# Kernel tuning notes

Hardware: AMD Instinct MI355X
Metric: run time of the kernel (lower is better)

## Reference

```python
import jax, jax.numpy as jnp
from jax import lax
import numpy as np

B, HW, C = 32, 4096, 256
G = 32            # factor / groups
CG = C // G       # per-group channels = 8
EPS = 1e-5


def setup_inputs() -> dict:
    key = jax.random.key(0)
    ks = jax.random.split(key, 7)
    s = 1.0 / np.sqrt(CG)
    s3 = 1.0 / np.sqrt(CG * 9)
    return {
        "x": jax.random.normal(ks[0], (B, HW, C), dtype=jnp.float32),
        "w1": jax.random.uniform(ks[1], (CG, CG), jnp.float32, -s, s),        # conv1x1 weight (O,I)
        "b1": jax.random.uniform(ks[2], (CG,), jnp.float32, -s, s),
        "w3": jax.random.uniform(ks[3], (CG, CG, 3, 3), jnp.float32, -s3, s3),  # conv3x3 weight (O,I,kH,kW)
        "b3": jax.random.uniform(ks[4], (CG,), jnp.float32, -s3, s3),
        "gn_w": jnp.ones((CG,), jnp.float32),
        "gn_b": jnp.zeros((CG,), jnp.float32),
    }


def reference(x, w1, b1, w3, b3, gn_w, gn_b):
    b, hw, c = x.shape
    h = int(np.sqrt(hw)); w = h
    cg = c // G
    n = b * G
    # (b, hw, c) -> (b, c, h, w) -> (b*G, cg, h, w)
    gx = x.transpose(0, 2, 1).reshape(b, c, h, w).reshape(n, cg, h, w)

    # directional pooling
    x_h = gx.mean(axis=3, keepdims=True)                       # (n,cg,h,1)
    x_w = gx.mean(axis=2, keepdims=True).transpose(0, 1, 3, 2)  # (n,cg,w,1)
    cat = jnp.concatenate([x_h, x_w], axis=2)                  # (n,cg,h+w,1)
    # 1x1 conv == channel matmul
    hwm = jnp.einsum('oi,nipq->nopq', w1, cat) + b1[None, :, None, None]
    xh, xw = hwm[:, :, :h], hwm[:, :, h:]

    gated = gx * jax.nn.sigmoid(xh) * jax.nn.sigmoid(xw.transpose(0, 1, 3, 2))

    # GroupNorm(cg groups over cg channels) == per-channel norm over spatial dims
    mu = gated.mean(axis=(2, 3), keepdims=True)
    var = gated.var(axis=(2, 3), keepdims=True)
    x1 = (gated - mu) * lax.rsqrt(var + EPS) * gn_w[None, :, None, None] + gn_b[None, :, None, None]

    x2 = lax.conv_general_dilated(gx, w3, (1, 1), ((1, 1), (1, 1)),
                                  dimension_numbers=('NCHW', 'OIHW', 'NCHW')) + b3[None, :, None, None]

    x11 = jax.nn.softmax(x1.mean(axis=(2, 3)), axis=-1)[:, None, :]  # (n,1,cg)
    x21 = jax.nn.softmax(x2.mean(axis=(2, 3)), axis=-1)[:, None, :]  # (n,1,cg)
    x12 = x2.reshape(n, cg, h * w)
    x22 = x1.reshape(n, cg, h * w)

    weights = (x11 @ x12 + x21 @ x22).reshape(n, 1, h, w)
    out = (gx * jax.nn.sigmoid(weights)).reshape(b, c, h, w)
    return out.reshape(b, c, hw).transpose(0, 2, 1)
```

## Files before the change

### kernel.cpp

```cpp
#include <hip/hip_runtime.h>
#include <math.h>


#define NBLK 1024
#define NTHR 512
#define CSTR 2052
#define USTR 4104

typedef unsigned int uint;
typedef unsigned short ushort;

__device__ __forceinline__ uint pk2(float a, float b) {
    uint ua = __builtin_bit_cast(uint, a);
    uint ub = __builtin_bit_cast(uint, b);
    ua = (ua + 0x7FFFu + ((ua >> 16) & 1u)) >> 16;
    ub = (ub + 0x7FFFu + ((ub >> 16) & 1u)) >> 16;
    return ua | (ub << 16);
}
__device__ __forceinline__ float blo(uint u) { return __builtin_bit_cast(float, u << 16); }
__device__ __forceinline__ float bhi(uint u) { return __builtin_bit_cast(float, u & 0xFFFF0000u); }
__device__ __forceinline__ float bfs(ushort s) { return __builtin_bit_cast(float, ((uint)s) << 16); }
__device__ __forceinline__ float sigm(float v) { return 1.0f / (1.0f + __expf(-v)); }
__device__ __forceinline__ uint pksig(float a, float b) {
    return (uint)(a * 65535.0f + 0.5f) | ((uint)(b * 65535.0f + 0.5f) << 16);
}

__global__ __launch_bounds__(512, 4) void fused_ema_kernel(
    const float* __restrict__ x,
    const float* __restrict__ w1,
    const float* __restrict__ b1,
    const float* __restrict__ w3,
    const float* __restrict__ b3,
    const float* __restrict__ gn_w,
    const float* __restrict__ gn_b,
    float* __restrict__ out)
{
    __shared__ __align__(16) uint  gxp[8 * CSTR];
    __shared__ __align__(16) float sg[8 * 128];
    __shared__ __align__(16) float uni[2048];
    __shared__ __align__(16) float t1s[8 * 64];
    __shared__ float weff[72];
    __shared__ float Ti[8], m2s[8], Ai[8], Ci[8], x11s[8], x21s[8];
    __shared__ float wconst_s;

    const int t = threadIdx.x;
    const int bi = blockIdx.x;
    const int n = ((bi & 7) * 32 + ((bi >> 3) >> 2)) * 4 + ((bi >> 3) & 3);
    const int b = n >> 5;
    const int g = n & 31;

    {
        const float4* x4 = reinterpret_cast<const float4*>(x) + (size_t)b * 4096 * 64 + g * 2;
#pragma unroll
        for (int k = 0; k < 8; ++k) {
            int idx = k * 512 + t;
            int q = idx >> 1;
            int half = idx & 1;
            float4 v0 = x4[(size_t)q * 128 + half];
            float4 v1 = x4[(size_t)q * 128 + 64 + half];
            int ch = half * 4;
            gxp[(ch + 0) * CSTR + q] = pk2(v0.x, v1.x);
            gxp[(ch + 1) * CSTR + q] = pk2(v0.y, v1.y);
            gxp[(ch + 2) * CSTR + q] = pk2(v0.z, v1.z);
            gxp[(ch + 3) * CSTR + q] = pk2(v0.w, v1.w);
        }
    }
    __syncthreads();

    float* Rs = uni;
    float* Cs = uni + 512;

    {
        const int i = t >> 6, l = t & 63, ys = l >> 3, xb = l & 7;
        float col[8] = {0, 0, 0, 0, 0, 0, 0, 0};
        float row[8];
#pragma unroll
        for (int r = 0; r < 8; ++r) {
            const uint4 d = *reinterpret_cast<const uint4*>(
                &gxp[i * CSTR + (ys * 8 + r) * 32 + xb * 4]);
            float f0 = blo(d.x), f1 = bhi(d.x), f2 = blo(d.y), f3 = bhi(d.y);
            float f4 = blo(d.z), f5 = bhi(d.z), f6 = blo(d.w), f7 = bhi(d.w);
            row[r] = ((f0 + f1) + (f2 + f3)) + ((f4 + f5) + (f6 + f7));
            col[0] += f0; col[1] += f1; col[2] += f2; col[3] += f3;
            col[4] += f4; col[5] += f5; col[6] += f6; col[7] += f7;
        }
#pragma unroll
        for (int r = 0; r < 8; ++r) {
            float v = row[r];
            v += __shfl_xor(v, 1); v += __shfl_xor(v, 2); v += __shfl_xor(v, 4);
            if (xb == 0) Rs[i * 64 + ys * 8 + r] = v;
        }
        float tot = 0.f;
#pragma unroll
        for (int j = 0; j < 8; ++j) {
            float c = col[j];
            c += __shfl_xor(c, 8); c += __shfl_xor(c, 16); c += __shfl_xor(c, 32);
            if (ys == 0) Cs[i * 64 + xb * 8 + j] = c;
            tot += c;
        }
        tot += __shfl_xor(tot, 1); tot += __shfl_xor(tot, 2); tot += __shfl_xor(tot, 4);
        if (l == 0) Ti[i] = tot;
    }
    __syncthreads();

    {
        const int o = t >> 6, p = t & 63;
        float vy = b1[o], vx = b1[o];
#pragma unroll
        for (int i = 0; i < 8; ++i) {
            float wv = w1[o * 8 + i] * (1.0f / 64.0f);
            vy += wv * Rs[i * 64 + p];
            vx += wv * Cs[i * 64 + p];
        }
        sg[o * 128 + p] = sigm(vy);
        sg[o * 128 + 64 + p] = sigm(vx);
    }
    __syncthreads();

    {
        const int i = t >> 6, l = t & 63, ys = l >> 3, xb = l & 7;
        const float4 sa = *reinterpret_cast<const float4*>(&sg[i * 128 + 64 + xb * 8]);
        const float4 sb = *reinterpret_cast<const float4*>(&sg[i * 128 + 64 + xb * 8 + 4]);
        float s = 0.f, s2 = 0.f;
#pragma unroll
        for (int r = 0; r < 8; ++r) {
            const float shv = sg[i * 128 + ys * 8 + r];
            const uint4 d = *reinterpret_cast<const uint4*>(
                &gxp[i * CSTR + (ys * 8 + r) * 32 + xb * 4]);
            float g0 = blo(d.x) * shv * sa.x; s += g0; s2 += g0 * g0;
            float g1 = bhi(d.x) * shv * sa.y; s += g1; s2 += g1 * g1;
            float g2 = blo(d.y) * shv * sa.z; s += g2; s2 += g2 * g2;
            float g3 = bhi(d.y) * shv * sa.w; s += g3; s2 += g3 * g3;
            float g4 = blo(d.z) * shv * sb.x; s += g4; s2 += g4 * g4;
            float g5 = bhi(d.z) * shv * sb.y; s += g5; s2 += g5 * g5;
            float g6 = blo(d.w) * shv * sb.z; s += g6; s2 += g6 * g6;
            float g7 = bhi(d.w) * shv * sb.w; s += g7; s2 += g7 * g7;
        }
#pragma unroll
        for (int off = 32; off; off >>= 1) {
            s += __shfl_xor(s, off);
            s2 += __shfl_xor(s2, off);
        }
        if (l == 0) {
            float mu = s * (1.0f / 4096.0f);
            float var = s2 * (1.0f / 4096.0f) - mu * mu;
            float a = rsqrtf(var + 1e-5f) * gn_w[i];
            Ai[i] = a;
            Ci[i] = gn_b[i] - mu * a;
        }
    }
    if (t < 64) {
        const int o = t >> 3, i = t & 7;
        const float T = Ti[i];
        float part = 0.f;
#pragma unroll
        for (int ky = 0; ky < 3; ++ky) {
            int dy = ky - 1;
#pragma unroll
            for (int kx = 0; kx < 3; ++kx) {
                int dx = kx - 1;
                float S = T;
                int er = (dy < 0) ? 63 : 0;
                int ec = (dx < 0) ? 63 : 0;
                if (dy != 0) S -= Rs[i * 64 + er];
                if (dx != 0) S -= Cs[i * 64 + ec];
                if (dy != 0 && dx != 0) {
                    uint u = gxp[i * CSTR + er * 32 + (ec >> 1)];
                    S += (ec & 1) ? bhi(u) : blo(u);
                }
                part += w3[((o * 8 + i) * 3 + ky) * 3 + kx] * S;
            }
        }
        part += __shfl_xor(part, 1); part += __shfl_xor(part, 2); part += __shfl_xor(part, 4);
        if (i == 0) m2s[o] = part * (1.0f / 4096.0f) + b3[o];
    }
    if (t < 8) {
        float mx = m2s[0];
#pragma unroll
        for (int o = 1; o < 8; ++o) mx = fmaxf(mx, m2s[o]);
        float sum = 0.f;
#pragma unroll
        for (int o = 0; o < 8; ++o) sum += __expf(m2s[o] - mx);
        x21s[t] = __expf(m2s[t] - mx) / sum;
        float mx1 = gn_b[0];
#pragma unroll
        for (int o = 1; o < 8; ++o) mx1 = fmaxf(mx1, gn_b[o]);
        float sum1 = 0.f;
#pragma unroll
        for (int o = 0; o < 8; ++o) sum1 += __expf(gn_b[o] - mx1);
        x11s[t] = __expf(gn_b[t] - mx1) / sum1;
    }
    __syncthreads();

    if (t < 72) {
        const int i = t / 9, k = t % 9;
        float acc = 0.f;
#pragma unroll
        for (int o = 0; o < 8; ++o) acc += x11s[o] * w3[(o * 8 + i) * 9 + k];
        weff[i * 9 + k] = acc;
    }
    {
        const int i = t >> 6, y = t & 63;
        t1s[i * 64 + y] = x21s[i] * Ai[i] * sg[i * 128 + y];
    }
    if (t == 0) {
        float wc = 0.f;
#pragma unroll
        for (int o = 0; o < 8; ++o) wc += x11s[o] * b3[o] + x21s[o] * Ci[o];
        wconst_s = wc;
    }
    __syncthreads();

    {
        const int y = t >> 3, xb = t & 7;
        const ushort* gxs = reinterpret_cast<const ushort*>(gxp);
        float ws0 = wconst_s, ws1 = ws0, ws2 = ws0, ws3 = ws0;
        float ws4 = ws0, ws5 = ws0, ws6 = ws0, ws7 = ws0;
#pragma unroll
        for (int i = 0; i < 8; ++i) {
            const float t1v = t1s[i * 64 + y];
            const float4 sa = *reinterpret_cast<const float4*>(&sg[i * 128 + 64 + xb * 8]);
            const float4 sb = *reinterpret_cast<const float4*>(&sg[i * 128 + 64 + xb * 8 + 4]);
            const int xm = (xb == 0) ? 0 : (xb * 8 - 1);
            const int xp = (xb == 7) ? 63 : (xb * 8 + 8);
#pragma unroll
            for (int dy = -1; dy <= 1; ++dy) {
                const int yy = y + dy;
                if (yy < 0 || yy > 63) continue;
                const uint4 d = *reinterpret_cast<const uint4*>(
                    &gxp[i * CSTR + yy * 32 + xb * 4]);
                float f0 = blo(d.x), f1 = bhi(d.x), f2 = blo(d.y), f3 = bhi(d.y);
                float f4 = blo(d.z), f5 = bhi(d.z), f6 = blo(d.w), f7 = bhi(d.w);
                float vm = (xb == 0) ? 0.f : bfs(gxs[i * USTR + yy * 64 + xm]);
                float vp = (xb == 7) ? 0.f : bfs(gxs[i * USTR + yy * 64 + xp]);
                const float* wp = &weff[i * 9 + (dy + 1) * 3];
                const float wl = wp[0], wc = wp[1], wr = wp[2];
                ws0 += wl * vm + wc * f0 + wr * f1;
                ws1 += wl * f0 + wc * f1 + wr * f2;
                ws2 += wl * f1 + wc * f2 + wr * f3;
                ws3 += wl * f2 + wc * f3 + wr * f4;
                ws4 += wl * f3 + wc * f4 + wr * f5;
                ws5 += wl * f4 + wc * f5 + wr * f6;
                ws6 += wl * f5 + wc * f6 + wr * f7;
                ws7 += wl * f6 + wc * f7 + wr * vp;
                if (dy == 0) {
                    ws0 += t1v * sa.x * f0;  ws1 += t1v * sa.y * f1;
                    ws2 += t1v * sa.z * f2;  ws3 += t1v * sa.w * f3;
                    ws4 += t1v * sb.x * f4;  ws5 += t1v * sb.y * f5;
                    ws6 += t1v * sb.z * f6;  ws7 += t1v * sb.w * f7;
                }
            }
        }
        uint* psum = reinterpret_cast<uint*>(uni);
        const int qb = y * 32 + xb * 4;
        psum[qb + 0] = pksig(sigm(ws0), sigm(ws1));
        psum[qb + 1] = pksig(sigm(ws2), sigm(ws3));
        psum[qb + 2] = pksig(sigm(ws4), sigm(ws5));
        psum[qb + 3] = pksig(sigm(ws6), sigm(ws7));
    }
    __syncthreads();

    {
        const uint* psum = reinterpret_cast<const uint*>(uni);
        float4* out4 = reinterpret_cast<float4*>(out) + (size_t)b * 4096 * 64 + g * 2;
#pragma unroll
        for (int j = 0; j < 4; ++j) {
            const int q = j * 512 + t;
            const uint sp = psum[q];
            const float s0 = (float)(sp & 0xFFFFu) * (1.0f / 65535.0f);
            const float s1 = (float)(sp >> 16) * (1.0f / 65535.0f);
            const uint u0 = gxp[0 * CSTR + q], u1 = gxp[1 * CSTR + q];
            const uint u2 = gxp[2 * CSTR + q], u3 = gxp[3 * CSTR + q];
            const uint u4 = gxp[4 * CSTR + q], u5 = gxp[5 * CSTR + q];
            const uint u6 = gxp[6 * CSTR + q], u7 = gxp[7 * CSTR + q];
            float4 a0, a1, c0, c1;
            a0.x = blo(u0) * s0; a0.y = blo(u1) * s0; a0.z = blo(u2) * s0; a0.w = blo(u3) * s0;
            a1.x = blo(u4) * s0; a1.y = blo(u5) * s0; a1.z = blo(u6) * s0; a1.w = blo(u7) * s0;
            c0.x = bhi(u0) * s1; c0.y = bhi(u1) * s1; c0.z = bhi(u2) * s1; c0.w = bhi(u3) * s1;
            c1.x = bhi(u4) * s1; c1.y = bhi(u5) * s1; c1.z = bhi(u6) * s1; c1.w = bhi(u7) * s1;
            const size_t p0 = (size_t)q * 128;
            out4[p0] = a0;
            out4[p0 + 1] = a1;
            out4[p0 + 64] = c0;
            out4[p0 + 65] = c1;
        }
    }
}

extern "C" void kernel_launch(void* const* d_in, const int* in_sizes, int n_in,
                              void* d_out, int out_size, void* d_ws, size_t ws_size,
                              hipStream_t stream) {
    const float* x    = (const float*)d_in[0];
    const float* w1   = (const float*)d_in[1];
    const float* b1   = (const float*)d_in[2];
    const float* w3   = (const float*)d_in[3];
    const float* b3   = (const float*)d_in[4];
    const float* gn_w = (const float*)d_in[5];
    const float* gn_b = (const float*)d_in[6];
    float* out = (float*)d_out;

    hipLaunchKernelGGL(fused_ema_kernel, dim3(NBLK), dim3(NTHR), 0, stream,
                       x, w1, b1, w3, b3, gn_w, gn_b, out);
}
```

Before: 89.53 us.

## Double threads per block and fuse conv output into final store

Raises the block size from 512 to 1024 threads so each thread covers 4 pixels instead of 8 in every phase, with a two-part column-sum and GroupNorm reduction across half-blocks. The 3x3 conv phase now takes left and right neighbours via wavefront shuffles instead of extra LDS loads, and keeps the centre row's data in registers so the output is written directly. This removes the packed-sigmoid LDS round-trip, its extra barrier and the 16-bit sigmoid quantisation. It adds barriers and reduction steps. The output store pattern changes from fully contiguous rows per warp to per-pixel strided float4 writes, which may hurt coalescing.

```diff
diff --git a/kernel.cpp b/kernel.cpp
--- a/kernel.cpp
+++ b/kernel.cpp
@@ -3,12 +3,10 @@
 
 
 #define NBLK 1024
-#define NTHR 512
+#define NTHR 1024
 #define CSTR 2052
-#define USTR 4104
 
 typedef unsigned int uint;
-typedef unsigned short ushort;
 
 __device__ __forceinline__ uint pk2(float a, float b) {
     uint ua = __builtin_bit_cast(uint, a);
@@ -19,13 +17,9 @@
 }
 __device__ __forceinline__ float blo(uint u) { return __builtin_bit_cast(float, u << 16); }
 __device__ __forceinline__ float bhi(uint u) { return __builtin_bit_cast(float, u & 0xFFFF0000u); }
-__device__ __forceinline__ float bfs(ushort s) { return __builtin_bit_cast(float, ((uint)s) << 16); }
 __device__ __forceinline__ float sigm(float v) { return 1.0f / (1.0f + __expf(-v)); }
-__device__ __forceinline__ uint pksig(float a, float b) {
-    return (uint)(a * 65535.0f + 0.5f) | ((uint)(b * 65535.0f + 0.5f) << 16);
-}
-
-__global__ __launch_bounds__(512, 4) void fused_ema_kernel(
+
+__global__ __launch_bounds__(1024, 8) void fused_ema_kernel(
     const float* __restrict__ x,
     const float* __restrict__ w1,
     const float* __restrict__ b1,
@@ -37,10 +31,12 @@
 {
     __shared__ __align__(16) uint  gxp[8 * CSTR];
     __shared__ __align__(16) float sg[8 * 128];
-    __shared__ __align__(16) float uni[2048];
-    __shared__ __align__(16) float t1s[8 * 64];
+    __shared__ __align__(16) float uni[1024];
+    __shared__ __align__(16) float csp1[512];
+    __shared__ __align__(16) float t1s[512];
     __shared__ float weff[72];
     __shared__ float Ti[8], m2s[8], Ai[8], Ci[8], x11s[8], x21s[8];
+    __shared__ float sPart[16], s2Part[16];
     __shared__ float wconst_s;
 
     const int t = threadIdx.x;
@@ -52,8 +48,8 @@
     {
         const float4* x4 = reinterpret_cast<const float4*>(x) + (size_t)b * 4096 * 64 + g * 2;
 #pragma unroll
-        for (int k = 0; k < 8; ++k) {
-            int idx = k * 512 + t;
+        for (int k = 0; k < 4; ++k) {
+            int idx = k * 1024 + t;
             int q = idx >> 1;
             int half = idx & 1;
             float4 v0 = x4[(size_t)q * 128 + half];
@@ -71,83 +67,90 @@
     float* Cs = uni + 512;
 
     {
-        const int i = t >> 6, l = t & 63, ys = l >> 3, xb = l & 7;
-        float col[8] = {0, 0, 0, 0, 0, 0, 0, 0};
-        float row[8];
+        const int i = t >> 7, l = t & 127;
+        const int ys2 = l >> 4, xb2 = l & 15;
+        float c0 = 0.f, c1 = 0.f, c2 = 0.f, c3 = 0.f;
+        float rowv[8];
 #pragma unroll
         for (int r = 0; r < 8; ++r) {
-            const uint4 d = *reinterpret_cast<const uint4*>(
-                &gxp[i * CSTR + (ys * 8 + r) * 32 + xb * 4]);
+            const uint2 d = *reinterpret_cast<const uint2*>(
+                &gxp[i * CSTR + (ys2 * 8 + r) * 32 + xb2 * 2]);
             float f0 = blo(d.x), f1 = bhi(d.x), f2 = blo(d.y), f3 = bhi(d.y);
-            float f4 = blo(d.z), f5 = bhi(d.z), f6 = blo(d.w), f7 = bhi(d.w);
-            row[r] = ((f0 + f1) + (f2 + f3)) + ((f4 + f5) + (f6 + f7));
-            col[0] += f0; col[1] += f1; col[2] += f2; col[3] += f3;
-            col[4] += f4; col[5] += f5; col[6] += f6; col[7] += f7;
+            rowv[r] = (f0 + f1) + (f2 + f3);
+            c0 += f0; c1 += f1; c2 += f2; c3 += f3;
         }
 #pragma unroll
         for (int r = 0; r < 8; ++r) {
-            float v = row[r];
-            v += __shfl_xor(v, 1); v += __shfl_xor(v, 2); v += __shfl_xor(v, 4);
-            if (xb == 0) Rs[i * 64 + ys * 8 + r] = v;
-        }
-        float tot = 0.f;
-#pragma unroll
-        for (int j = 0; j < 8; ++j) {
-            float c = col[j];
-            c += __shfl_xor(c, 8); c += __shfl_xor(c, 16); c += __shfl_xor(c, 32);
-            if (ys == 0) Cs[i * 64 + xb * 8 + j] = c;
-            tot += c;
-        }
-        tot += __shfl_xor(tot, 1); tot += __shfl_xor(tot, 2); tot += __shfl_xor(tot, 4);
-        if (l == 0) Ti[i] = tot;
-    }
-    __syncthreads();
-
-    {
-        const int o = t >> 6, p = t & 63;
-        float vy = b1[o], vx = b1[o];
+            float v = rowv[r];
+            v += __shfl_xor(v, 1); v += __shfl_xor(v, 2);
+            v += __shfl_xor(v, 4); v += __shfl_xor(v, 8);
+            if (xb2 == 0) Rs[i * 64 + ys2 * 8 + r] = v;
+        }
+        c0 += __shfl_xor(c0, 16); c0 += __shfl_xor(c0, 32);
+        c1 += __shfl_xor(c1, 16); c1 += __shfl_xor(c1, 32);
+        c2 += __shfl_xor(c2, 16); c2 += __shfl_xor(c2, 32);
+        c3 += __shfl_xor(c3, 16); c3 += __shfl_xor(c3, 32);
+        if ((l & 63) < 16) {
+            float* dst = (l < 64) ? &Cs[i * 64 + xb2 * 4] : &csp1[i * 64 + xb2 * 4];
+            *reinterpret_cast<float4*>(dst) = make_float4(c0, c1, c2, c3);
+        }
+    }
+    __syncthreads();
+    if (t < 512) {
+        const int i = t >> 6, j = t & 63;
+        float c = Cs[t] + csp1[t];
+        Cs[t] = c;
+        float s = c;
+#pragma unroll
+        for (int off = 32; off; off >>= 1) s += __shfl_xor(s, off);
+        if (j == 0) Ti[i] = s;
+    }
+    __syncthreads();
+
+    {
+        const int o = t >> 7, p = t & 127;
+        float val = b1[o];
 #pragma unroll
         for (int i = 0; i < 8; ++i) {
-            float wv = w1[o * 8 + i] * (1.0f / 64.0f);
-            vy += wv * Rs[i * 64 + p];
-            vx += wv * Cs[i * 64 + p];
-        }
-        sg[o * 128 + p] = sigm(vy);
-        sg[o * 128 + 64 + p] = sigm(vx);
-    }
-    __syncthreads();
-
-    {
-        const int i = t >> 6, l = t & 63, ys = l >> 3, xb = l & 7;
-        const float4 sa = *reinterpret_cast<const float4*>(&sg[i * 128 + 64 + xb * 8]);
-        const float4 sb = *reinterpret_cast<const float4*>(&sg[i * 128 + 64 + xb * 8 + 4]);
+            float cv = (p < 64) ? Rs[i * 64 + p] : Cs[i * 64 + (p - 64)];
+            val += w1[o * 8 + i] * (cv * (1.0f / 64.0f));
+        }
+        sg[o * 128 + p] = sigm(val);
+    }
+    __syncthreads();
+
+    {
+        const int i = t >> 7, l = t & 127;
+        const int ys2 = l >> 4, xb2 = l & 15;
+        const float4 sa = *reinterpret_cast<const float4*>(&sg[i * 128 + 64 + xb2 * 4]);
         float s = 0.f, s2 = 0.f;
 #pragma unroll
         for (int r = 0; r < 8; ++r) {
-            const float shv = sg[i * 128 + ys * 8 + r];
-            const uint4 d = *reinterpret_cast<const uint4*>(
-                &gxp[i * CSTR + (ys * 8 + r) * 32 + xb * 4]);
+            const float shv = sg[i * 128 + ys2 * 8 + r];
+            const uint2 d = *reinterpret_cast<const uint2*>(
+                &gxp[i * CSTR + (ys2 * 8 + r) * 32 + xb2 * 2]);
             float g0 = blo(d.x) * shv * sa.x; s += g0; s2 += g0 * g0;
             float g1 = bhi(d.x) * shv * sa.y; s += g1; s2 += g1 * g1;
             float g2 = blo(d.y) * shv * sa.z; s += g2; s2 += g2 * g2;
             float g3 = bhi(d.y) * shv * sa.w; s += g3; s2 += g3 * g3;
-            float g4 = blo(d.z) * shv * sb.x; s += g4; s2 += g4 * g4;
-            float g5 = bhi(d.z) * shv * sb.y; s += g5; s2 += g5 * g5;
-            float g6 = blo(d.w) * shv * sb.z; s += g6; s2 += g6 * g6;
-            float g7 = bhi(d.w) * shv * sb.w; s += g7; s2 += g7 * g7;
         }
 #pragma unroll
         for (int off = 32; off; off >>= 1) {
             s += __shfl_xor(s, off);
             s2 += __shfl_xor(s2, off);
         }
-        if (l == 0) {
-            float mu = s * (1.0f / 4096.0f);
-            float var = s2 * (1.0f / 4096.0f) - mu * mu;
-            float a = rsqrtf(var + 1e-5f) * gn_w[i];
-            Ai[i] = a;
-            Ci[i] = gn_b[i] - mu * a;
-        }
+        if ((t & 63) == 0) { sPart[t >> 6] = s; s2Part[t >> 6] = s2; }
+    }
+    __syncthreads();
+
+    if (t < 8) {
+        float s  = sPart[2 * t] + sPart[2 * t + 1];
+        float s2 = s2Part[2 * t] + s2Part[2 * t + 1];
+        float mu = s * (1.0f / 4096.0f);
+        float var = s2 * (1.0f / 4096.0f) - mu * mu;
+        float a = rsqrtf(var + 1e-5f) * gn_w[t];
+        Ai[t] = a;
+        Ci[t] = gn_b[t] - mu * a;
     }
     if (t < 64) {
         const int o = t >> 3, i = t & 7;
@@ -199,7 +202,7 @@
         for (int o = 0; o < 8; ++o) acc += x11s[o] * w3[(o * 8 + i) * 9 + k];
         weff[i * 9 + k] = acc;
     }
-    {
+    if (t < 512) {
         const int i = t >> 6, y = t & 63;
         t1s[i * 64 + y] = x21s[i] * Ai[i] * sg[i * 128 + y];
     }
@@ -212,78 +215,55 @@
     __syncthreads();
 
     {
-        const int y = t >> 3, xb = t & 7;
-        const ushort* gxs = reinterpret_cast<const ushort*>(gxp);
-        float ws0 = wconst_s, ws1 = ws0, ws2 = ws0, ws3 = ws0;
-        float ws4 = ws0, ws5 = ws0, ws6 = ws0, ws7 = ws0;
+        const int y = t >> 4, xq = t & 15;
+        const bool xl = (xq == 0), xr = (xq == 15);
+        float ws0 = wconst_s, ws1 = wconst_s, ws2 = wconst_s, ws3 = wconst_s;
+        uint2 gg[8];
 #pragma unroll
         for (int i = 0; i < 8; ++i) {
             const float t1v = t1s[i * 64 + y];
-            const float4 sa = *reinterpret_cast<const float4*>(&sg[i * 128 + 64 + xb * 8]);
-            const float4 sb = *reinterpret_cast<const float4*>(&sg[i * 128 + 64 + xb * 8 + 4]);
-            const int xm = (xb == 0) ? 0 : (xb * 8 - 1);
-            const int xp = (xb == 7) ? 63 : (xb * 8 + 8);
+            const float4 sa = *reinterpret_cast<const float4*>(&sg[i * 128 + 64 + xq * 4]);
 #pragma unroll
             for (int dy = -1; dy <= 1; ++dy) {
                 const int yy = y + dy;
                 if (yy < 0 || yy > 63) continue;
-                const uint4 d = *reinterpret_cast<const uint4*>(
-                    &gxp[i * CSTR + yy * 32 + xb * 4]);
+                const uint2 d = *reinterpret_cast<const uint2*>(
+                    &gxp[i * CSTR + yy * 32 + xq * 2]);
                 float f0 = blo(d.x), f1 = bhi(d.x), f2 = blo(d.y), f3 = bhi(d.y);
-                float f4 = blo(d.z), f5 = bhi(d.z), f6 = blo(d.w), f7 = bhi(d.w);
-                float vm = (xb == 0) ? 0.f : bfs(gxs[i * USTR + yy * 64 + xm]);
-                float vp = (xb == 7) ? 0.f : bfs(gxs[i * USTR + yy * 64 + xp]);
-                const float* wp = &weff[i * 9 + (dy + 1) * 3];
-                const float wl = wp[0], wc = wp[1], wr = wp[2];
+                float vm = __shfl_up(f3, 1);
+                float vp = __shfl_down(f0, 1);
+                vm = xl ? 0.f : vm;
+                vp = xr ? 0.f : vp;
+                const float wl = weff[i * 9 + (dy + 1) * 3 + 0];
+                const float wc = weff[i * 9 + (dy + 1) * 3 + 1];
+                const float wr = weff[i * 9 + (dy + 1) * 3 + 2];
                 ws0 += wl * vm + wc * f0 + wr * f1;
                 ws1 += wl * f0 + wc * f1 + wr * f2;
                 ws2 += wl * f1 + wc * f2 + wr * f3;
-                ws3 += wl * f2 + wc * f3 + wr * f4;
-                ws4 += wl * f3 + wc * f4 + wr * f5;
-                ws5 += wl * f4 + wc * f5 + wr * f6;
-                ws6 += wl * f5 + wc * f6 + wr * f7;
-                ws7 += wl * f6 + wc * f7 + wr * vp;
+                ws3 += wl * f2 + wc * f3 + wr * vp;
                 if (dy == 0) {
+                    gg[i] = d;
                     ws0 += t1v * sa.x * f0;  ws1 += t1v * sa.y * f1;
                     ws2 += t1v * sa.z * f2;  ws3 += t1v * sa.w * f3;
-                    ws4 += t1v * sb.x * f4;  ws5 += t1v * sb.y * f5;
-                    ws6 += t1v * sb.z * f6;  ws7 += t1v * sb.w * f7;
                 }
             }
         }
-        uint* psum = reinterpret_cast<uint*>(uni);
-        const int qb = y * 32 + xb * 4;
-        psum[qb + 0] = pksig(sigm(ws0), sigm(ws1));
-        psum[qb + 1] = pksig(sigm(ws2), sigm(ws3));
-        psum[qb + 2] = pksig(sigm(ws4), sigm(ws5));
-        psum[qb + 3] = pksig(sigm(ws6), sigm(ws7));
-    }
-    __syncthreads();
-
-    {
-        const uint* psum = reinterpret_cast<const uint*>(uni);
+        const float s0 = sigm(ws0), s1 = sigm(ws1), s2 = sigm(ws2), s3 = sigm(ws3);
         float4* out4 = reinterpret_cast<float4*>(out) + (size_t)b * 4096 * 64 + g * 2;
-#pragma unroll
-        for (int j = 0; j < 4; ++j) {
-            const int q = j * 512 + t;
-            const uint sp = psum[q];
-            const float s0 = (float)(sp & 0xFFFFu) * (1.0f / 65535.0f);
-            const float s1 = (float)(sp >> 16) * (1.0f / 65535.0f);
-            const uint u0 = gxp[0 * CSTR + q], u1 = gxp[1 * CSTR + q];
-            const uint u2 = gxp[2 * CSTR + q], u3 = gxp[3 * CSTR + q];
-            const uint u4 = gxp[4 * CSTR + q], u5 = gxp[5 * CSTR + q];
-            const uint u6 = gxp[6 * CSTR + q], u7 = gxp[7 * CSTR + q];
-            float4 a0, a1, c0, c1;
-            a0.x = blo(u0) * s0; a0.y = blo(u1) * s0; a0.z = blo(u2) * s0; a0.w = blo(u3) * s0;
-            a1.x = blo(u4) * s0; a1.y = blo(u5) * s0; a1.z = blo(u6) * s0; a1.w = blo(u7) * s0;
-            c0.x = bhi(u0) * s1; c0.y = bhi(u1) * s1; c0.z = bhi(u2) * s1; c0.w = bhi(u3) * s1;
-            c1.x = bhi(u4) * s1; c1.y = bhi(u5) * s1; c1.z = bhi(u6) * s1; c1.w = bhi(u7) * s1;
-            const size_t p0 = (size_t)q * 128;
-            out4[p0] = a0;
-            out4[p0 + 1] = a1;
-            out4[p0 + 64] = c0;
-            out4[p0 + 65] = c1;
-        }
+        const size_t pb = (size_t)(y * 64 + xq * 4) * 64;
+        float4 lo, hi;
+        lo.x = blo(gg[0].x) * s0; lo.y = blo(gg[1].x) * s0; lo.z = blo(gg[2].x) * s0; lo.w = blo(gg[3].x) * s0;
+        hi.x = blo(gg[4].x) * s0; hi.y = blo(gg[5].x) * s0; hi.z = blo(gg[6].x) * s0; hi.w = blo(gg[7].x) * s0;
+        out4[pb + 0] = lo; out4[pb + 1] = hi;
+        lo.x = bhi(gg[0].x) * s1; lo.y = bhi(gg[1].x) * s1; lo.z = bhi(gg[2].x) * s1; lo.w = bhi(gg[3].x) * s1;
+        hi.x = bhi(gg[4].x) * s1; hi.y = bhi(gg[5].x) * s1; hi.z = bhi(gg[6].x) * s1; hi.w = bhi(gg[7].x) * s1;
+        out4[pb + 64] = lo; out4[pb + 65] = hi;
+        lo.x = blo(gg[0].y) * s2; lo.y = blo(gg[1].y) * s2; lo.z = blo(gg[2].y) * s2; lo.w = blo(gg[3].y) * s2;
+        hi.x = blo(gg[4].y) * s2; hi.y = blo(gg[5].y) * s2; hi.z = blo(gg[6].y) * s2; hi.w = blo(gg[7].y) * s2;
+        out4[pb + 128] = lo; out4[pb + 129] = hi;
+        lo.x = bhi(gg[0].y) * s3; lo.y = bhi(gg[1].y) * s3; lo.z = bhi(gg[2].y) * s3; lo.w = bhi(gg[3].y) * s3;
+        hi.x = bhi(gg[4].y) * s3; hi.y = bhi(gg[5].y) * s3; hi.z = bhi(gg[6].y) * s3; hi.w = bhi(gg[7].y) * s3;
+        out4[pb + 192] = lo; out4[pb + 193] = hi;
     }
 }
 
```

Measured after the change: 106.5 us. 18.9% more time.

## Fuse output write into stencil stage using register-held tiles and shuffles

Applied to the files above, without the earlier changes.

Halo neighbours for the 3x3 stencil now come from lane shuffles (shfl_up/down), replacing scalar LDS loads. The conv weights are padded to float4 rows so they load as vectors. Each thread keeps its centre-row bf16 data in registers and writes the gated output directly. This removes the quantized sigmoid staging buffer, a barrier and the final LDS re-read pass. The cost is more registers, since 8 uint4 plus the accumulators stay live, and the stores are less coalesced: each thread writes 8 pixels at a 64-float4 stride.

```diff
diff --git a/kernel.cpp b/kernel.cpp
--- a/kernel.cpp
+++ b/kernel.cpp
@@ -5,10 +5,8 @@
 #define NBLK 1024
 #define NTHR 512
 #define CSTR 2052
-#define USTR 4104
 
 typedef unsigned int uint;
-typedef unsigned short ushort;
 
 __device__ __forceinline__ uint pk2(float a, float b) {
     uint ua = __builtin_bit_cast(uint, a);
@@ -19,11 +17,7 @@
 }
 __device__ __forceinline__ float blo(uint u) { return __builtin_bit_cast(float, u << 16); }
 __device__ __forceinline__ float bhi(uint u) { return __builtin_bit_cast(float, u & 0xFFFF0000u); }
-__device__ __forceinline__ float bfs(ushort s) { return __builtin_bit_cast(float, ((uint)s) << 16); }
 __device__ __forceinline__ float sigm(float v) { return 1.0f / (1.0f + __expf(-v)); }
-__device__ __forceinline__ uint pksig(float a, float b) {
-    return (uint)(a * 65535.0f + 0.5f) | ((uint)(b * 65535.0f + 0.5f) << 16);
-}
 
 __global__ __launch_bounds__(512, 4) void fused_ema_kernel(
     const float* __restrict__ x,
@@ -37,9 +31,9 @@
 {
     __shared__ __align__(16) uint  gxp[8 * CSTR];
     __shared__ __align__(16) float sg[8 * 128];
-    __shared__ __align__(16) float uni[2048];
-    __shared__ __align__(16) float t1s[8 * 64];
-    __shared__ float weff[72];
+    __shared__ __align__(16) float uni[1024];
+    __shared__ __align__(16) float t1s[512];
+    __shared__ __align__(16) float weff[96];
     __shared__ float Ti[8], m2s[8], Ai[8], Ci[8], x11s[8], x21s[8];
     __shared__ float wconst_s;
 
@@ -73,20 +67,20 @@
     {
         const int i = t >> 6, l = t & 63, ys = l >> 3, xb = l & 7;
         float col[8] = {0, 0, 0, 0, 0, 0, 0, 0};
-        float row[8];
+        float rowv[8];
 #pragma unroll
         for (int r = 0; r < 8; ++r) {
             const uint4 d = *reinterpret_cast<const uint4*>(
                 &gxp[i * CSTR + (ys * 8 + r) * 32 + xb * 4]);
             float f0 = blo(d.x), f1 = bhi(d.x), f2 = blo(d.y), f3 = bhi(d.y);
             float f4 = blo(d.z), f5 = bhi(d.z), f6 = blo(d.w), f7 = bhi(d.w);
-            row[r] = ((f0 + f1) + (f2 + f3)) + ((f4 + f5) + (f6 + f7));
+            rowv[r] = ((f0 + f1) + (f2 + f3)) + ((f4 + f5) + (f6 + f7));
             col[0] += f0; col[1] += f1; col[2] += f2; col[3] += f3;
             col[4] += f4; col[5] += f5; col[6] += f6; col[7] += f7;
         }
 #pragma unroll
         for (int r = 0; r < 8; ++r) {
-            float v = row[r];
+            float v = rowv[r];
             v += __shfl_xor(v, 1); v += __shfl_xor(v, 2); v += __shfl_xor(v, 4);
             if (xb == 0) Rs[i * 64 + ys * 8 + r] = v;
         }
@@ -197,7 +191,7 @@
         float acc = 0.f;
 #pragma unroll
         for (int o = 0; o < 8; ++o) acc += x11s[o] * w3[(o * 8 + i) * 9 + k];
-        weff[i * 9 + k] = acc;
+        weff[i * 12 + (k / 3) * 4 + (k % 3)] = acc;
     }
     {
         const int i = t >> 6, y = t & 63;
@@ -213,16 +207,14 @@
 
     {
         const int y = t >> 3, xb = t & 7;
-        const ushort* gxs = reinterpret_cast<const ushort*>(gxp);
-        float ws0 = wconst_s, ws1 = ws0, ws2 = ws0, ws3 = ws0;
-        float ws4 = ws0, ws5 = ws0, ws6 = ws0, ws7 = ws0;
+        float ws0 = wconst_s, ws1 = wconst_s, ws2 = wconst_s, ws3 = wconst_s;
+        float ws4 = wconst_s, ws5 = wconst_s, ws6 = wconst_s, ws7 = wconst_s;
+        uint4 gla[8];
 #pragma unroll
         for (int i = 0; i < 8; ++i) {
             const float t1v = t1s[i * 64 + y];
             const float4 sa = *reinterpret_cast<const float4*>(&sg[i * 128 + 64 + xb * 8]);
             const float4 sb = *reinterpret_cast<const float4*>(&sg[i * 128 + 64 + xb * 8 + 4]);
-            const int xm = (xb == 0) ? 0 : (xb * 8 - 1);
-            const int xp = (xb == 7) ? 63 : (xb * 8 + 8);
 #pragma unroll
             for (int dy = -1; dy <= 1; ++dy) {
                 const int yy = y + dy;
@@ -231,10 +223,12 @@
                     &gxp[i * CSTR + yy * 32 + xb * 4]);
                 float f0 = blo(d.x), f1 = bhi(d.x), f2 = blo(d.y), f3 = bhi(d.y);
                 float f4 = blo(d.z), f5 = bhi(d.z), f6 = blo(d.w), f7 = bhi(d.w);
-                float vm = (xb == 0) ? 0.f : bfs(gxs[i * USTR + yy * 64 + xm]);
-                float vp = (xb == 7) ? 0.f : bfs(gxs[i * USTR + yy * 64 + xp]);
-                const float* wp = &weff[i * 9 + (dy + 1) * 3];
-                const float wl = wp[0], wc = wp[1], wr = wp[2];
+                float vm = __shfl_up(f7, 1);
+                float vp = __shfl_down(f0, 1);
+                vm = (xb == 0) ? 0.f : vm;
+                vp = (xb == 7) ? 0.f : vp;
+                const float4 wv = *reinterpret_cast<const float4*>(&weff[i * 12 + (dy + 1) * 4]);
+                const float wl = wv.x, wc = wv.y, wr = wv.z;
                 ws0 += wl * vm + wc * f0 + wr * f1;
                 ws1 += wl * f0 + wc * f1 + wr * f2;
                 ws2 += wl * f1 + wc * f2 + wr * f3;
@@ -244,6 +238,7 @@
                 ws6 += wl * f5 + wc * f6 + wr * f7;
                 ws7 += wl * f6 + wc * f7 + wr * vp;
                 if (dy == 0) {
+                    gla[i] = d;
                     ws0 += t1v * sa.x * f0;  ws1 += t1v * sa.y * f1;
                     ws2 += t1v * sa.z * f2;  ws3 += t1v * sa.w * f3;
                     ws4 += t1v * sb.x * f4;  ws5 += t1v * sb.y * f5;
@@ -251,39 +246,35 @@
                 }
             }
         }
-        uint* psum = reinterpret_cast<uint*>(uni);
-        const int qb = y * 32 + xb * 4;
-        psum[qb + 0] = pksig(sigm(ws0), sigm(ws1));
-        psum[qb + 1] = pksig(sigm(ws2), sigm(ws3));
-        psum[qb + 2] = pksig(sigm(ws4), sigm(ws5));
-        psum[qb + 3] = pksig(sigm(ws6), sigm(ws7));
-    }
-    __syncthreads();
-
-    {
-        const uint* psum = reinterpret_cast<const uint*>(uni);
+        const float s0 = sigm(ws0), s1 = sigm(ws1), s2 = sigm(ws2), s3 = sigm(ws3);
+        const float s4 = sigm(ws4), s5 = sigm(ws5), s6 = sigm(ws6), s7 = sigm(ws7);
         float4* out4 = reinterpret_cast<float4*>(out) + (size_t)b * 4096 * 64 + g * 2;
-#pragma unroll
-        for (int j = 0; j < 4; ++j) {
-            const int q = j * 512 + t;
-            const uint sp = psum[q];
-            const float s0 = (float)(sp & 0xFFFFu) * (1.0f / 65535.0f);
-            const float s1 = (float)(sp >> 16) * (1.0f / 65535.0f);
-            const uint u0 = gxp[0 * CSTR + q], u1 = gxp[1 * CSTR + q];
-            const uint u2 = gxp[2 * CSTR + q], u3 = gxp[3 * CSTR + q];
-            const uint u4 = gxp[4 * CSTR + q], u5 = gxp[5 * CSTR + q];
-            const uint u6 = gxp[6 * CSTR + q], u7 = gxp[7 * CSTR + q];
-            float4 a0, a1, c0, c1;
-            a0.x = blo(u0) * s0; a0.y = blo(u1) * s0; a0.z = blo(u2) * s0; a0.w = blo(u3) * s0;
-            a1.x = blo(u4) * s0; a1.y = blo(u5) * s0; a1.z = blo(u6) * s0; a1.w = blo(u7) * s0;
-            c0.x = bhi(u0) * s1; c0.y = bhi(u1) * s1; c0.z = bhi(u2) * s1; c0.w = bhi(u3) * s1;
-            c1.x = bhi(u4) * s1; c1.y = bhi(u5) * s1; c1.z = bhi(u6) * s1; c1.w = bhi(u7) * s1;
-            const size_t p0 = (size_t)q * 128;
-            out4[p0] = a0;
-            out4[p0 + 1] = a1;
-            out4[p0 + 64] = c0;
-            out4[p0 + 65] = c1;
-        }
+        const size_t pb = (size_t)(y * 64 + xb * 8) * 64;
+        float4 lo, hi;
+        lo.x = blo(gla[0].x) * s0; lo.y = blo(gla[1].x) * s0; lo.z = blo(gla[2].x) * s0; lo.w = blo(gla[3].x) * s0;
+        hi.x = blo(gla[4].x) * s0; hi.y = blo(gla[5].x) * s0; hi.z = blo(gla[6].x) * s0; hi.w = blo(gla[7].x) * s0;
+        out4[pb + 0] = lo; out4[pb + 1] = hi;
+        lo.x = bhi(gla[0].x) * s1; lo.y = bhi(gla[1].x) * s1; lo.z = bhi(gla[2].x) * s1; lo.w = bhi(gla[3].x) * s1;
+        hi.x = bhi(gla[4].x) * s1; hi.y = bhi(gla[5].x) * s1; hi.z = bhi(gla[6].x) * s1; hi.w = bhi(gla[7].x) * s1;
+        out4[pb + 64] = lo; out4[pb + 65] = hi;
+        lo.x = blo(gla[0].y) * s2; lo.y = blo(gla[1].y) * s2; lo.z = blo(gla[2].y) * s2; lo.w = blo(gla[3].y) * s2;
+        hi.x = blo(gla[4].y) * s2; hi.y = blo(gla[5].y) * s2; hi.z = blo(gla[6].y) * s2; hi.w = blo(gla[7].y) * s2;
+        out4[pb + 128] = lo; out4[pb + 129] = hi;
+        lo.x = bhi(gla[0].y) * s3; lo.y = bhi(gla[1].y) * s3; lo.z = bhi(gla[2].y) * s3; lo.w = bhi(gla[3].y) * s3;
+        hi.x = bhi(gla[4].y) * s3; hi.y = bhi(gla[5].y) * s3; hi.z = bhi(gla[6].y) * s3; hi.w = bhi(gla[7].y) * s3;
+        out4[pb + 192] = lo; out4[pb + 193] = hi;
+        lo.x = blo(gla[0].z) * s4; lo.y = blo(gla[1].z) * s4; lo.z = blo(gla[2].z) * s4; lo.w = blo(gla[3].z) * s4;
+        hi.x = blo(gla[4].z) * s4; hi.y = blo(gla[5].z) * s4; hi.z = blo(gla[6].z) * s4; hi.w = blo(gla[7].z) * s4;
+        out4[pb + 256] = lo; out4[pb + 257] = hi;
+        lo.x = bhi(gla[0].z) * s5; lo.y = bhi(gla[1].z) * s5; lo.z = bhi(gla[2].z) * s5; lo.w = bhi(gla[3].z) * s5;
+        hi.x = bhi(gla[4].z) * s5; hi.y = bhi(gla[5].z) * s5; hi.z = bhi(gla[6].z) * s5; hi.w = bhi(gla[7].z) * s5;
+        out4[pb + 320] = lo; out4[pb + 321] = hi;
+        lo.x = blo(gla[0].w) * s6; lo.y = blo(gla[1].w) * s6; lo.z = blo(gla[2].w) * s6; lo.w = blo(gla[3].w) * s6;
+        hi.x = blo(gla[4].w) * s6; hi.y = blo(gla[5].w) * s6; hi.z = blo(gla[6].w) * s6; hi.w = blo(gla[7].w) * s6;
+        out4[pb + 384] = lo; out4[pb + 385] = hi;
+        lo.x = bhi(gla[0].w) * s7; lo.y = bhi(gla[1].w) * s7; lo.z = bhi(gla[2].w) * s7; lo.w = bhi(gla[3].w) * s7;
+        hi.x = bhi(gla[4].w) * s7; hi.y = bhi(gla[5].w) * s7; hi.z = bhi(gla[6].w) * s7; hi.w = bhi(gla[7].w) * s7;
+        out4[pb + 448] = lo; out4[pb + 449] = hi;
     }
 }
 
```

New measurement: 82.94 us. -7.4%, faster.
